# Kernel tuning notes

Hardware: AMD Instinct MI355X
Metric: run time of the kernel (lower is better)

## Reference

```python
import jax, jax.numpy as jnp
import numpy as np


def setup_inputs() -> dict:
    key = jax.random.key(0)
    k1, k2 = jax.random.split(key)
    querry_emb = jax.random.normal(k1, (4096, 1024), dtype=jnp.float32)
    traj_emb = jax.random.normal(k2, (8192, 1024), dtype=jnp.float32)
    return {"querry_emb": querry_emb, "traj_emb": traj_emb}


def reference(querry_emb, traj_emb):
    # Cosine-similarity score: (Q K^T) / (|q| outer |k|)  -> [Nq, Nk]
    q_norm = jnp.sqrt(jnp.sum(querry_emb * querry_emb, axis=1))  # [Nq]
    k_norm = jnp.sqrt(jnp.sum(traj_emb * traj_emb, axis=1))      # [Nk]
    score = jnp.einsum('qd,kd->qk', querry_emb, traj_emb) / (q_norm[:, None] * k_norm[None, :])
    # Softmax over key axis (torch dim=1 on [Nq, Nk])
    atten = jax.nn.softmax(score, axis=1)
    # Context: weighted sum of values (traj_emb)
    context = jnp.einsum('qk,kd->qd', atten, traj_emb)
    return context
```

## Files before the change

### kernel.cpp

```cpp
#include <hip/hip_runtime.h>

#define NQ 4096
#define NK 8192
#define DIM 1024

typedef __attribute__((ext_vector_type(8))) short short8;
typedef __attribute__((ext_vector_type(4))) float floatx4;
typedef unsigned int u32;
typedef __attribute__((address_space(3))) u32 lds_u32;
typedef __attribute__((address_space(1))) const u32 glb_u32;

__device__ __forceinline__ void gload_lds16(const void* g, void* l) {
    __builtin_amdgcn_global_load_lds((glb_u32*)g, (lds_u32*)l, 16, 0, 0);
}

__device__ __forceinline__ unsigned short f32_bf16(float f) {
    unsigned int u = __float_as_uint(f);
    u += 0x7fff + ((u >> 16) & 1);
    return (unsigned short)(u >> 16);
}

__device__ __forceinline__ void tile_body(const unsigned short* A0,
                                          const unsigned short* B0,
                                          int ar, int br,
                                          floatx4 (&acc)[8][4]) {
    short8 a[4], b[4];
#pragma unroll
    for (int nj = 0; nj < 4; ++nj)
        b[nj] = *(const short8*)&B0[br + nj * 512];
#pragma unroll
    for (int mi = 0; mi < 4; ++mi)
        a[mi] = *(const short8*)&A0[ar + mi * 512];
    __builtin_amdgcn_s_setprio(1);
#pragma unroll
    for (int mi = 0; mi < 4; ++mi)
#pragma unroll
        for (int nj = 0; nj < 4; ++nj)
            acc[mi][nj] = __builtin_amdgcn_mfma_f32_16x16x32_bf16(b[nj], a[mi], acc[mi][nj], 0, 0, 0);
    __builtin_amdgcn_s_setprio(0);
#pragma unroll
    for (int mi = 0; mi < 4; ++mi)
        a[mi] = *(const short8*)&A0[ar + 2048 + mi * 512];
    __builtin_amdgcn_s_setprio(1);
#pragma unroll
    for (int mi = 0; mi < 4; ++mi)
#pragma unroll
        for (int nj = 0; nj < 4; ++nj)
            acc[4 + mi][nj] = __builtin_amdgcn_mfma_f32_16x16x32_bf16(b[nj], a[mi], acc[4 + mi][nj], 0, 0, 0);
    __builtin_amdgcn_s_setprio(0);
}

__global__ void prep_q_zero(const float* __restrict__ Q,
                            unsigned short* __restrict__ Qb,
                            float* __restrict__ inv_qn,
                            float* __restrict__ lsum,
                            float* __restrict__ out_zero) {
    int wave = threadIdx.x >> 6;
    int lane = threadIdx.x & 63;
    int row  = blockIdx.x * 4 + wave;
    const float* r = Q + (size_t)row * DIM;
    float s = 0.f;
#pragma unroll
    for (int c = 0; c < 4; ++c) {
        float4 f = *(const float4*)(r + c * 256 + lane * 4);
        s += f.x * f.x + f.y * f.y + f.z * f.z + f.w * f.w;
        ushort4 b;
        b.x = f32_bf16(f.x); b.y = f32_bf16(f.y);
        b.z = f32_bf16(f.z); b.w = f32_bf16(f.w);
        *(ushort4*)(Qb + (size_t)row * DIM + c * 256 + lane * 4) = b;
    }
#pragma unroll
    for (int off = 32; off > 0; off >>= 1) s += __shfl_xor(s, off);
    if (lane == 0) inv_qn[row] = 1.0f / sqrtf(s);

    float4 z = make_float4(0.f, 0.f, 0.f, 0.f);
    if (out_zero) {
#pragma unroll
        for (int c = 0; c < 4; ++c)
            *(float4*)(out_zero + (size_t)blockIdx.x * 4096 + c * 1024 + threadIdx.x * 4) = z;
    }
    if (blockIdx.x < 4)
        *(float4*)(lsum + blockIdx.x * 1024 + threadIdx.x * 4) = z;
}

__global__ void prep_norm_cvt(const float* __restrict__ src,
                              unsigned short* __restrict__ dst,
                              float* __restrict__ inv_norm) {
    int wave = threadIdx.x >> 6;
    int lane = threadIdx.x & 63;
    int row  = blockIdx.x * 4 + wave;
    const float* r = src + (size_t)row * DIM;
    float s = 0.f;
#pragma unroll
    for (int c = 0; c < 4; ++c) {
        float4 f = *(const float4*)(r + c * 256 + lane * 4);
        s += f.x * f.x + f.y * f.y + f.z * f.z + f.w * f.w;
        ushort4 b;
        b.x = f32_bf16(f.x); b.y = f32_bf16(f.y);
        b.z = f32_bf16(f.z); b.w = f32_bf16(f.w);
        *(ushort4*)(dst + (size_t)row * DIM + c * 256 + lane * 4) = b;
    }
#pragma unroll
    for (int off = 32; off > 0; off >>= 1) s += __shfl_xor(s, off);
    if (lane == 0) inv_norm[row] = 1.0f / sqrtf(s);
}

__global__ void transpose_cvt(const float* __restrict__ K,
                              unsigned short* __restrict__ Kt) {
    __shared__ float t[64][65];
    int kn0 = blockIdx.x * 64, d0 = blockIdx.y * 64;
    int tid = threadIdx.x;
    int r  = tid >> 4;
    int c4 = (tid & 15) * 4;
#pragma unroll
    for (int s = 0; s < 4; ++s) {
        int kk = s * 16 + r;
        float4 f = *(const float4*)(K + (size_t)(kn0 + kk) * DIM + d0 + c4);
        t[kk][c4 + 0] = f.x; t[kk][c4 + 1] = f.y;
        t[kk][c4 + 2] = f.z; t[kk][c4 + 3] = f.w;
    }
    __syncthreads();
#pragma unroll
    for (int s = 0; s < 4; ++s) {
        int dd = s * 16 + r;
        ushort4 b;
        b.x = f32_bf16(t[c4 + 0][dd]);
        b.y = f32_bf16(t[c4 + 1][dd]);
        b.z = f32_bf16(t[c4 + 2][dd]);
        b.w = f32_bf16(t[c4 + 3][dd]);
        *(ushort4*)(Kt + (size_t)(d0 + dd) * NK + kn0 + c4) = b;
    }
}

__global__ __launch_bounds__(512, 2) void score_gemm(
        const unsigned short* __restrict__ Qb,
        const unsigned short* __restrict__ Kb,
        const float* __restrict__ inv_qn,
        const float* __restrict__ inv_kn,
        unsigned short* __restrict__ P,
        float* __restrict__ lsum) {
    __shared__ __align__(16) unsigned short A_lds[4][256 * 32];
    __shared__ __align__(16) unsigned short B_lds[4][256 * 32];

    int bid = blockIdx.x;
    int swz = (bid & 7) * 64 + (bid >> 3);
    int q0  = (swz & 15) * 256;
    int n0  = (swz >> 4) * 256;

    int tid  = threadIdx.x;
    int wave = tid >> 6, lane = tid & 63;
    int wm = wave >> 2, wn = wave & 3;
    int quad = lane >> 4, l16 = lane & 15;
    int rcol = (quad ^ ((l16 >> 1) & 3)) * 8;

    int schunk = ((tid & 3) ^ ((tid >> 3) & 3)) * 8;
    const unsigned short* gA = Qb + (size_t)(q0 + (tid >> 2)) * DIM + schunk;
    const unsigned short* gB = Kb + (size_t)(n0 + (tid >> 2)) * DIM + schunk;

#define STG(t1)                                                       \
    do {                                                              \
        const unsigned short* _ga = gA + (t1) * 32;                   \
        const unsigned short* _gb = gB + (t1) * 32;                   \
        unsigned short* _la = &A_lds[(t1) & 3][wave * 512];           \
        unsigned short* _lb = &B_lds[(t1) & 3][wave * 512];           \
        gload_lds16(_ga, _la);                                        \
        gload_lds16(_ga + (size_t)128 * DIM, _la + 4096);             \
        gload_lds16(_gb, _lb);                                        \
        gload_lds16(_gb + (size_t)128 * DIM, _lb + 4096);             \
    } while (0)

    floatx4 acc[8][4];
#pragma unroll
    for (int i = 0; i < 8; ++i)
#pragma unroll
        for (int j = 0; j < 4; ++j) acc[i][j] = (floatx4)(0.0f);

    const int ar = (wm * 128 + l16) * 32 + rcol;
    const int br = (wn * 64 + l16) * 32 + rcol;

    STG(0); STG(1); STG(2);

#pragma unroll 4
    for (int t = 0; t < 28; ++t) {
        asm volatile("s_waitcnt vmcnt(8)" ::: "memory");
        __builtin_amdgcn_s_barrier();
        STG(t + 3);
        tile_body(&A_lds[t & 3][0], &B_lds[t & 3][0], ar, br, acc);
    }
    asm volatile("s_waitcnt vmcnt(8)" ::: "memory");
    __builtin_amdgcn_s_barrier();
    STG(31);
    tile_body(&A_lds[0][0], &B_lds[0][0], ar, br, acc);
    asm volatile("s_waitcnt vmcnt(8)" ::: "memory");
    __builtin_amdgcn_s_barrier();
    tile_body(&A_lds[1][0], &B_lds[1][0], ar, br, acc);
    asm volatile("s_waitcnt vmcnt(4)" ::: "memory");
    __builtin_amdgcn_s_barrier();
    tile_body(&A_lds[2][0], &B_lds[2][0], ar, br, acc);
    asm volatile("s_waitcnt vmcnt(0)" ::: "memory");
    __builtin_amdgcn_s_barrier();
    tile_body(&A_lds[3][0], &B_lds[3][0], ar, br, acc);
#undef STG

#pragma unroll
    for (int i = 0; i < 8; ++i) {
        int qrow = q0 + wm * 128 + i * 16 + l16;
        float iqn = inv_qn[qrow];
        float rs = 0.f;
#pragma unroll
        for (int j = 0; j < 4; ++j) {
            int ncol = n0 + wn * 64 + j * 16 + quad * 4;
            float4 ik = *(const float4*)&inv_kn[ncol];
            float p0 = __expf(acc[i][j][0] * iqn * ik.x);
            float p1 = __expf(acc[i][j][1] * iqn * ik.y);
            float p2 = __expf(acc[i][j][2] * iqn * ik.z);
            float p3 = __expf(acc[i][j][3] * iqn * ik.w);
            ushort4 pb;
            pb.x = f32_bf16(p0); pb.y = f32_bf16(p1);
            pb.z = f32_bf16(p2); pb.w = f32_bf16(p3);
            *(ushort4*)&P[(size_t)qrow * NK + ncol] = pb;
            rs += p0 + p1 + p2 + p3;
        }
        rs += __shfl_xor(rs, 16);
        rs += __shfl_xor(rs, 32);
        if (quad == 0) atomicAdd(&lsum[qrow], rs);
    }
}

__global__ __launch_bounds__(512, 2) void ctx_gemm_st(
        const unsigned short* __restrict__ P,
        const unsigned short* __restrict__ Kt,
        float* __restrict__ part) {
    __shared__ __align__(16) unsigned short A_lds[4][256 * 32];
    __shared__ __align__(16) unsigned short B_lds[4][256 * 32];

    int bid = blockIdx.x;
    int swz = (bid & 7) * 32 + (bid >> 3);
    int z  = swz >> 6;
    int y  = (swz >> 2) & 15;
    int x  = swz & 3;
    int q0 = y * 256;
    int d0 = x * 256;
    int kbase = z * (NK / 4);

    int tid  = threadIdx.x;
    int wave = tid >> 6, lane = tid & 63;
    int wm = wave >> 2, wn = wave & 3;
    int quad = lane >> 4, l16 = lane & 15;
    int rcol = (quad ^ ((l16 >> 1) & 3)) * 8;

    int schunk = ((tid & 3) ^ ((tid >> 3) & 3)) * 8;
    const unsigned short* gA = P  + (size_t)(q0 + (tid >> 2)) * NK + kbase + schunk;
    const unsigned short* gB = Kt + (size_t)(d0 + (tid >> 2)) * NK + kbase + schunk;

#define STG(t1)                                                       \
    do {                                                              \
        const unsigned short* _ga = gA + (t1) * 32;                   \
        const unsigned short* _gb = gB + (t1) * 32;                   \
        unsigned short* _la = &A_lds[(t1) & 3][wave * 512];           \
        unsigned short* _lb = &B_lds[(t1) & 3][wave * 512];           \
        gload_lds16(_ga, _la);                                        \
        gload_lds16(_ga + (size_t)128 * NK, _la + 4096);              \
        gload_lds16(_gb, _lb);                                        \
        gload_lds16(_gb + (size_t)128 * NK, _lb + 4096);              \
    } while (0)

    floatx4 acc[8][4];
#pragma unroll
    for (int i = 0; i < 8; ++i)
#pragma unroll
        for (int j = 0; j < 4; ++j) acc[i][j] = (floatx4)(0.0f);

    const int ar = (wm * 128 + l16) * 32 + rcol;
    const int br = (wn * 64 + l16) * 32 + rcol;

    STG(0); STG(1); STG(2);

#pragma unroll 4
    for (int t = 0; t < 60; ++t) {
        asm volatile("s_waitcnt vmcnt(8)" ::: "memory");
        __builtin_amdgcn_s_barrier();
        STG(t + 3);
        tile_body(&A_lds[t & 3][0], &B_lds[t & 3][0], ar, br, acc);
    }
    asm volatile("s_waitcnt vmcnt(8)" ::: "memory");
    __builtin_amdgcn_s_barrier();
    STG(63);
    tile_body(&A_lds[0][0], &B_lds[0][0], ar, br, acc);
    asm volatile("s_waitcnt vmcnt(8)" ::: "memory");
    __builtin_amdgcn_s_barrier();
    tile_body(&A_lds[1][0], &B_lds[1][0], ar, br, acc);
    asm volatile("s_waitcnt vmcnt(4)" ::: "memory");
    __builtin_amdgcn_s_barrier();
    tile_body(&A_lds[2][0], &B_lds[2][0], ar, br, acc);
    asm volatile("s_waitcnt vmcnt(0)" ::: "memory");
    __builtin_amdgcn_s_barrier();
    tile_body(&A_lds[3][0], &B_lds[3][0], ar, br, acc);
#undef STG

    float* pslice = part + (size_t)z * NQ * DIM;
#pragma unroll
    for (int i = 0; i < 8; ++i) {
        int qrow = q0 + wm * 128 + i * 16 + l16;
#pragma unroll
        for (int j = 0; j < 4; ++j) {
            int dcol = d0 + wn * 64 + j * 16 + quad * 4;
            float4 v;
            v.x = acc[i][j][0]; v.y = acc[i][j][1];
            v.z = acc[i][j][2]; v.w = acc[i][j][3];
            *(float4*)&pslice[(size_t)qrow * DIM + dcol] = v;
        }
    }
}

__global__ void reduce_out(const float* __restrict__ part,
                           const float* __restrict__ lsum,
                           float* __restrict__ out) {
    size_t idx = ((size_t)blockIdx.x * 256 + threadIdx.x) * 4;
    int q = (int)(idx >> 10);
    float inv = 1.0f / lsum[q];
    const size_t S = (size_t)NQ * DIM;
    float4 s0 = *(const float4*)(part + idx);
    float4 s1 = *(const float4*)(part + S + idx);
    float4 s2 = *(const float4*)(part + 2 * S + idx);
    float4 s3 = *(const float4*)(part + 3 * S + idx);
    float4 o;
    o.x = (s0.x + s1.x + s2.x + s3.x) * inv;
    o.y = (s0.y + s1.y + s2.y + s3.y) * inv;
    o.z = (s0.z + s1.z + s2.z + s3.z) * inv;
    o.w = (s0.w + s1.w + s2.w + s3.w) * inv;
    *(float4*)(out + idx) = o;
}

__global__ void ctx_gemm(const unsigned short* __restrict__ P,
                         const unsigned short* __restrict__ Kt,
                         const float* __restrict__ lsum,
                         float* __restrict__ out) {
    __shared__ __align__(16) unsigned short As[128 * 32];
    __shared__ __align__(16) unsigned short Bs[128 * 32];
    int id = blockIdx.x;
    int r8 = id & 7;
    int t  = id >> 3;
    int x  = t & 7;
    int g  = ((t >> 3) << 3) | r8;
    int y  = g & 31;
    int z  = g >> 5;
    int q0 = y * 128;
    int d0 = x * 128;
    int kbase = z * (NK / 4);

    int tid = threadIdx.x;
    int wave = tid >> 6, lane = tid & 63;
    int wm = wave >> 1, wn = wave & 1;
    int quad = lane >> 4, l16 = lane & 15;

    int srow   = wave * 32 + (lane >> 2);
    int schunk = (((lane & 3) ^ ((lane >> 3) & 3))) * 8;
    const unsigned short* gA0 = P + (size_t)(q0 + srow) * NK + kbase + schunk;
    const unsigned short* gA1 = gA0 + (size_t)16 * NK;
    const unsigned short* gB0 = Kt + (size_t)(d0 + srow) * NK + kbase + schunk;
    const unsigned short* gB1 = gB0 + (size_t)16 * NK;
    unsigned short* lA0 = As + wave * 32 * 32;
    unsigned short* lA1 = lA0 + 16 * 32;
    unsigned short* lB0 = Bs + wave * 32 * 32;
    unsigned short* lB1 = lB0 + 16 * 32;

    int rcol = (quad ^ ((l16 >> 1) & 3)) * 8;

    floatx4 acc[4][4];
#pragma unroll
    for (int i = 0; i < 4; ++i)
#pragma unroll
        for (int j = 0; j < 4; ++j) acc[i][j] = (floatx4)(0.0f);

    for (int kb = 0; kb < (NK / 4) / 32; ++kb) {
        int k0 = kb * 32;
        __syncthreads();
        gload_lds16(gA0 + k0, lA0);
        gload_lds16(gA1 + k0, lA1);
        gload_lds16(gB0 + k0, lB0);
        gload_lds16(gB1 + k0, lB1);
        __syncthreads();
        short8 a[4], b[4];
#pragma unroll
        for (int i = 0; i < 4; ++i)
            a[i] = *(const short8*)&As[(wm * 64 + i * 16 + l16) * 32 + rcol];
#pragma unroll
        for (int j = 0; j < 4; ++j)
            b[j] = *(const short8*)&Bs[(wn * 64 + j * 16 + l16) * 32 + rcol];
#pragma unroll
        for (int i = 0; i < 4; ++i)
#pragma unroll
            for (int j = 0; j < 4; ++j)
                acc[i][j] = __builtin_amdgcn_mfma_f32_16x16x32_bf16(a[i], b[j], acc[i][j], 0, 0, 0);
    }

#pragma unroll
    for (int i = 0; i < 4; ++i) {
        float invl[4];
#pragma unroll
        for (int r = 0; r < 4; ++r)
            invl[r] = 1.0f / lsum[q0 + wm * 64 + i * 16 + quad * 4 + r];
#pragma unroll
        for (int j = 0; j < 4; ++j) {
#pragma unroll
            for (int r = 0; r < 4; ++r) {
                int qrow = q0 + wm * 64 + i * 16 + quad * 4 + r;
                int dcol = d0 + wn * 64 + j * 16 + l16;
                atomicAdd(&out[(size_t)qrow * DIM + dcol], acc[i][j][r] * invl[r]);
            }
        }
    }
}

__global__ void fused_fallback(const float* __restrict__ Q,
                               const float* __restrict__ K,
                               float* __restrict__ out) {
    int wave = threadIdx.x >> 6, lane = threadIdx.x & 63;
    int q0 = blockIdx.x * 16 + wave * 4;
    float qv[4][16], acc[4][16], iqn[4], ls[4];
#pragma unroll
    for (int r = 0; r < 4; ++r) {
        float s = 0.f;
#pragma unroll
        for (int c = 0; c < 4; ++c) {
            float4 f = *(const float4*)(Q + (size_t)(q0 + r) * DIM + c * 256 + lane * 4);
            qv[r][c * 4 + 0] = f.x; qv[r][c * 4 + 1] = f.y;
            qv[r][c * 4 + 2] = f.z; qv[r][c * 4 + 3] = f.w;
            s += f.x * f.x + f.y * f.y + f.z * f.z + f.w * f.w;
        }
#pragma unroll
        for (int off = 32; off > 0; off >>= 1) s += __shfl_xor(s, off);
        iqn[r] = 1.0f / sqrtf(s);
        ls[r] = 0.f;
#pragma unroll
        for (int t = 0; t < 16; ++t) acc[r][t] = 0.f;
    }
    for (int k = 0; k < NK; ++k) {
        const float* kr = K + (size_t)k * DIM;
        float kv[16], ss = 0.f;
#pragma unroll
        for (int c = 0; c < 4; ++c) {
            float4 f = *(const float4*)(kr + c * 256 + lane * 4);
            kv[c * 4 + 0] = f.x; kv[c * 4 + 1] = f.y;
            kv[c * 4 + 2] = f.z; kv[c * 4 + 3] = f.w;
            ss += f.x * f.x + f.y * f.y + f.z * f.z + f.w * f.w;
        }
        float d0 = 0.f, d1 = 0.f, d2 = 0.f, d3 = 0.f;
#pragma unroll
        for (int t = 0; t < 16; ++t) {
            d0 += qv[0][t] * kv[t]; d1 += qv[1][t] * kv[t];
            d2 += qv[2][t] * kv[t]; d3 += qv[3][t] * kv[t];
        }
#pragma unroll
        for (int off = 32; off > 0; off >>= 1) {
            ss += __shfl_xor(ss, off);
            d0 += __shfl_xor(d0, off); d1 += __shfl_xor(d1, off);
            d2 += __shfl_xor(d2, off); d3 += __shfl_xor(d3, off);
        }
        float ikn = 1.0f / sqrtf(ss);
        float p0 = __expf(d0 * iqn[0] * ikn), p1 = __expf(d1 * iqn[1] * ikn);
        float p2 = __expf(d2 * iqn[2] * ikn), p3 = __expf(d3 * iqn[3] * ikn);
        ls[0] += p0; ls[1] += p1; ls[2] += p2; ls[3] += p3;
#pragma unroll
        for (int t = 0; t < 16; ++t) {
            acc[0][t] += p0 * kv[t]; acc[1][t] += p1 * kv[t];
            acc[2][t] += p2 * kv[t]; acc[3][t] += p3 * kv[t];
        }
    }
#pragma unroll
    for (int r = 0; r < 4; ++r) {
        float inv = 1.0f / ls[r];
#pragma unroll
        for (int c = 0; c < 4; ++c) {
            float4 o;
            o.x = acc[r][c * 4 + 0] * inv; o.y = acc[r][c * 4 + 1] * inv;
            o.z = acc[r][c * 4 + 2] * inv; o.w = acc[r][c * 4 + 3] * inv;
            *(float4*)(out + (size_t)(q0 + r) * DIM + c * 256 + lane * 4) = o;
        }
    }
}

extern "C" void kernel_launch(void* const* d_in, const int* in_sizes, int n_in,
                              void* d_out, int out_size, void* d_ws, size_t ws_size,
                              hipStream_t stream) {
    const float* Q = (const float*)d_in[0];
    const float* K = (const float*)d_in[1];
    float* out = (float*)d_out;
    char* ws = (char*)d_ws;

    const size_t REQ_T1 = ((size_t)152u << 20) + 65536;
    const size_t REQ_T2 = ((size_t)88u << 20) + 65536;

    if (ws_size >= REQ_T1) {
        unsigned short* Kt = (unsigned short*)(ws);
        unsigned short* Qb = (unsigned short*)(ws);
        unsigned short* Kb = (unsigned short*)(ws + (size_t)(8u << 20));
        unsigned short* P  = (unsigned short*)(ws + (size_t)(24u << 20));
        float* part   = (float*)(ws + (size_t)(88u << 20));
        float* inv_qn = (float*)(ws + (size_t)(152u << 20));
        float* inv_kn = (float*)(ws + (size_t)(152u << 20) + 16384);
        float* lsum   = (float*)(ws + (size_t)(152u << 20) + 49152);

        prep_q_zero<<<NQ / 4, 256, 0, stream>>>(Q, Qb, inv_qn, lsum, nullptr);
        prep_norm_cvt<<<NK / 4, 256, 0, stream>>>(K, Kb, inv_kn);
        score_gemm<<<512, 512, 0, stream>>>(Qb, Kb, inv_qn, inv_kn, P, lsum);
        transpose_cvt<<<dim3(NK / 64, DIM / 64), 256, 0, stream>>>(K, Kt);
        ctx_gemm_st<<<256, 512, 0, stream>>>(P, Kt, part);
        reduce_out<<<NQ * DIM / 1024, 256, 0, stream>>>(part, lsum, out);
    } else if (ws_size >= REQ_T2) {
        unsigned short* Kt = (unsigned short*)(ws);
        unsigned short* Qb = (unsigned short*)(ws);
        unsigned short* Kb = (unsigned short*)(ws + (size_t)(8u << 20));
        unsigned short* P  = (unsigned short*)(ws + (size_t)(24u << 20));
        float* inv_qn = (float*)(ws + (size_t)(88u << 20));
        float* inv_kn = (float*)(ws + (size_t)(88u << 20) + 16384);
        float* lsum   = (float*)(ws + (size_t)(88u << 20) + 49152);

        prep_q_zero<<<NQ / 4, 256, 0, stream>>>(Q, Qb, inv_qn, lsum, out);
        prep_norm_cvt<<<NK / 4, 256, 0, stream>>>(K, Kb, inv_kn);
        score_gemm<<<512, 512, 0, stream>>>(Qb, Kb, inv_qn, inv_kn, P, lsum);
        transpose_cvt<<<dim3(NK / 64, DIM / 64), 256, 0, stream>>>(K, Kt);
        ctx_gemm<<<1024, 256, 0, stream>>>(P, Kt, lsum, out);
    } else {
        fused_fallback<<<NQ / 16, 256, 0, stream>>>(Q, K, out);
    }
}
```

Baseline: 263.7 us.

## Shrink GEMM block tiles to 128x256 with double buffering and more blocks

Score and context GEMMs move from 256x256 tiles with a 4-stage LDS pipeline to 128x256 tiles with a 2-stage pipeline. This halves accumulator registers and LDS per block, allowing launch bounds of 4 blocks per CU and doubling the grid sizes. The goal is more occupancy and better CU load balance. The trade-offs are lower data reuse per tile, more global traffic for B, and a full vmcnt(0) wait each iteration that shortens prefetch depth.

```diff
diff --git a/kernel.cpp b/kernel.cpp
--- a/kernel.cpp
+++ b/kernel.cpp
@@ -18,36 +18,6 @@
     unsigned int u = __float_as_uint(f);
     u += 0x7fff + ((u >> 16) & 1);
     return (unsigned short)(u >> 16);
-}
-
-__device__ __forceinline__ void tile_body(const unsigned short* A0,
-                                          const unsigned short* B0,
-                                          int ar, int br,
-                                          floatx4 (&acc)[8][4]) {
-    short8 a[4], b[4];
-#pragma unroll
-    for (int nj = 0; nj < 4; ++nj)
-        b[nj] = *(const short8*)&B0[br + nj * 512];
-#pragma unroll
-    for (int mi = 0; mi < 4; ++mi)
-        a[mi] = *(const short8*)&A0[ar + mi * 512];
-    __builtin_amdgcn_s_setprio(1);
-#pragma unroll
-    for (int mi = 0; mi < 4; ++mi)
-#pragma unroll
-        for (int nj = 0; nj < 4; ++nj)
-            acc[mi][nj] = __builtin_amdgcn_mfma_f32_16x16x32_bf16(b[nj], a[mi], acc[mi][nj], 0, 0, 0);
-    __builtin_amdgcn_s_setprio(0);
-#pragma unroll
-    for (int mi = 0; mi < 4; ++mi)
-        a[mi] = *(const short8*)&A0[ar + 2048 + mi * 512];
-    __builtin_amdgcn_s_setprio(1);
-#pragma unroll
-    for (int mi = 0; mi < 4; ++mi)
-#pragma unroll
-        for (int nj = 0; nj < 4; ++nj)
-            acc[4 + mi][nj] = __builtin_amdgcn_mfma_f32_16x16x32_bf16(b[nj], a[mi], acc[4 + mi][nj], 0, 0, 0);
-    __builtin_amdgcn_s_setprio(0);
 }
 
 __global__ void prep_q_zero(const float* __restrict__ Q,
@@ -132,20 +102,20 @@
     }
 }
 
-__global__ __launch_bounds__(512, 2) void score_gemm(
+__global__ __launch_bounds__(512, 4) void score_gemm(
         const unsigned short* __restrict__ Qb,
         const unsigned short* __restrict__ Kb,
         const float* __restrict__ inv_qn,
         const float* __restrict__ inv_kn,
         unsigned short* __restrict__ P,
         float* __restrict__ lsum) {
-    __shared__ __align__(16) unsigned short A_lds[4][256 * 32];
-    __shared__ __align__(16) unsigned short B_lds[4][256 * 32];
+    __shared__ __align__(16) unsigned short A_lds[2][128 * 32];
+    __shared__ __align__(16) unsigned short B_lds[2][256 * 32];
 
     int bid = blockIdx.x;
-    int swz = (bid & 7) * 64 + (bid >> 3);
-    int q0  = (swz & 15) * 256;
-    int n0  = (swz >> 4) * 256;
+    int swz = (bid & 7) * 128 + (bid >> 3);
+    int q0  = (swz & 31) * 128;
+    int n0  = (swz >> 5) * 256;
 
     int tid  = threadIdx.x;
     int wave = tid >> 6, lane = tid & 63;
@@ -159,52 +129,49 @@
 
 #define STG(t1)                                                       \
     do {                                                              \
-        const unsigned short* _ga = gA + (t1) * 32;                   \
-        const unsigned short* _gb = gB + (t1) * 32;                   \
-        unsigned short* _la = &A_lds[(t1) & 3][wave * 512];           \
-        unsigned short* _lb = &B_lds[(t1) & 3][wave * 512];           \
-        gload_lds16(_ga, _la);                                        \
-        gload_lds16(_ga + (size_t)128 * DIM, _la + 4096);             \
-        gload_lds16(_gb, _lb);                                        \
-        gload_lds16(_gb + (size_t)128 * DIM, _lb + 4096);             \
+        gload_lds16(gA + (t1) * 32, &A_lds[(t1) & 1][wave * 512]);    \
+        gload_lds16(gB + (t1) * 32, &B_lds[(t1) & 1][wave * 512]);    \
+        gload_lds16(gB + (size_t)128 * DIM + (t1) * 32,               \
+                    &B_lds[(t1) & 1][wave * 512 + 4096]);             \
     } while (0)
 
-    floatx4 acc[8][4];
-#pragma unroll
-    for (int i = 0; i < 8; ++i)
+    floatx4 acc[4][4];
+#pragma unroll
+    for (int i = 0; i < 4; ++i)
 #pragma unroll
         for (int j = 0; j < 4; ++j) acc[i][j] = (floatx4)(0.0f);
 
-    const int ar = (wm * 128 + l16) * 32 + rcol;
+    const int ar = (wm * 64 + l16) * 32 + rcol;
     const int br = (wn * 64 + l16) * 32 + rcol;
-
-    STG(0); STG(1); STG(2);
-
-#pragma unroll 4
-    for (int t = 0; t < 28; ++t) {
-        asm volatile("s_waitcnt vmcnt(8)" ::: "memory");
+    const int NT = DIM / 32;
+
+    STG(0);
+#pragma unroll 2
+    for (int t = 0; t < NT; ++t) {
+        asm volatile("s_waitcnt vmcnt(0)" ::: "memory");
         __builtin_amdgcn_s_barrier();
-        STG(t + 3);
-        tile_body(&A_lds[t & 3][0], &B_lds[t & 3][0], ar, br, acc);
-    }
-    asm volatile("s_waitcnt vmcnt(8)" ::: "memory");
-    __builtin_amdgcn_s_barrier();
-    STG(31);
-    tile_body(&A_lds[0][0], &B_lds[0][0], ar, br, acc);
-    asm volatile("s_waitcnt vmcnt(8)" ::: "memory");
-    __builtin_amdgcn_s_barrier();
-    tile_body(&A_lds[1][0], &B_lds[1][0], ar, br, acc);
-    asm volatile("s_waitcnt vmcnt(4)" ::: "memory");
-    __builtin_amdgcn_s_barrier();
-    tile_body(&A_lds[2][0], &B_lds[2][0], ar, br, acc);
-    asm volatile("s_waitcnt vmcnt(0)" ::: "memory");
-    __builtin_amdgcn_s_barrier();
-    tile_body(&A_lds[3][0], &B_lds[3][0], ar, br, acc);
+        if (t + 1 < NT) STG(t + 1);
+        const unsigned short* Ab = &A_lds[t & 1][0];
+        const unsigned short* Bb = &B_lds[t & 1][0];
+        short8 b[4];
+#pragma unroll
+        for (int nj = 0; nj < 4; ++nj)
+            b[nj] = *(const short8*)&Bb[br + nj * 512];
+        __builtin_amdgcn_s_setprio(1);
+#pragma unroll
+        for (int mi = 0; mi < 4; ++mi) {
+            short8 a = *(const short8*)&Ab[ar + mi * 512];
+#pragma unroll
+            for (int nj = 0; nj < 4; ++nj)
+                acc[mi][nj] = __builtin_amdgcn_mfma_f32_16x16x32_bf16(b[nj], a, acc[mi][nj], 0, 0, 0);
+        }
+        __builtin_amdgcn_s_setprio(0);
+    }
 #undef STG
 
 #pragma unroll
-    for (int i = 0; i < 8; ++i) {
-        int qrow = q0 + wm * 128 + i * 16 + l16;
+    for (int i = 0; i < 4; ++i) {
+        int qrow = q0 + wm * 64 + i * 16 + l16;
         float iqn = inv_qn[qrow];
         float rs = 0.f;
 #pragma unroll
@@ -227,19 +194,20 @@
     }
 }
 
-__global__ __launch_bounds__(512, 2) void ctx_gemm_st(
+__global__ __launch_bounds__(512, 4) void ctx_gemm_st(
         const unsigned short* __restrict__ P,
         const unsigned short* __restrict__ Kt,
         float* __restrict__ part) {
-    __shared__ __align__(16) unsigned short A_lds[4][256 * 32];
-    __shared__ __align__(16) unsigned short B_lds[4][256 * 32];
+    __shared__ __align__(16) unsigned short A_lds[2][128 * 32];
+    __shared__ __align__(16) unsigned short B_lds[2][256 * 32];
 
     int bid = blockIdx.x;
-    int swz = (bid & 7) * 32 + (bid >> 3);
-    int z  = swz >> 6;
-    int y  = (swz >> 2) & 15;
-    int x  = swz & 3;
-    int q0 = y * 256;
+    int swz = (bid & 7) * 64 + (bid >> 3);
+    int z  = swz >> 7;
+    int rem = swz & 127;
+    int y  = rem >> 2;
+    int x  = rem & 3;
+    int q0 = y * 128;
     int d0 = x * 256;
     int kbase = z * (NK / 4);
 
@@ -255,53 +223,50 @@
 
 #define STG(t1)                                                       \
     do {                                                              \
-        const unsigned short* _ga = gA + (t1) * 32;                   \
-        const unsigned short* _gb = gB + (t1) * 32;                   \
-        unsigned short* _la = &A_lds[(t1) & 3][wave * 512];           \
-        unsigned short* _lb = &B_lds[(t1) & 3][wave * 512];           \
-        gload_lds16(_ga, _la);                                        \
-        gload_lds16(_ga + (size_t)128 * NK, _la + 4096);              \
-        gload_lds16(_gb, _lb);                                        \
-        gload_lds16(_gb + (size_t)128 * NK, _lb + 4096);              \
+        gload_lds16(gA + (t1) * 32, &A_lds[(t1) & 1][wave * 512]);    \
+        gload_lds16(gB + (t1) * 32, &B_lds[(t1) & 1][wave * 512]);    \
+        gload_lds16(gB + (size_t)128 * NK + (t1) * 32,                \
+                    &B_lds[(t1) & 1][wave * 512 + 4096]);             \
     } while (0)
 
-    floatx4 acc[8][4];
-#pragma unroll
-    for (int i = 0; i < 8; ++i)
+    floatx4 acc[4][4];
+#pragma unroll
+    for (int i = 0; i < 4; ++i)
 #pragma unroll
         for (int j = 0; j < 4; ++j) acc[i][j] = (floatx4)(0.0f);
 
-    const int ar = (wm * 128 + l16) * 32 + rcol;
+    const int ar = (wm * 64 + l16) * 32 + rcol;
     const int br = (wn * 64 + l16) * 32 + rcol;
-
-    STG(0); STG(1); STG(2);
-
-#pragma unroll 4
-    for (int t = 0; t < 60; ++t) {
-        asm volatile("s_waitcnt vmcnt(8)" ::: "memory");
+    const int NT = (NK / 4) / 32;
+
+    STG(0);
+#pragma unroll 2
+    for (int t = 0; t < NT; ++t) {
+        asm volatile("s_waitcnt vmcnt(0)" ::: "memory");
         __builtin_amdgcn_s_barrier();
-        STG(t + 3);
-        tile_body(&A_lds[t & 3][0], &B_lds[t & 3][0], ar, br, acc);
-    }
-    asm volatile("s_waitcnt vmcnt(8)" ::: "memory");
-    __builtin_amdgcn_s_barrier();
-    STG(63);
-    tile_body(&A_lds[0][0], &B_lds[0][0], ar, br, acc);
-    asm volatile("s_waitcnt vmcnt(8)" ::: "memory");
-    __builtin_amdgcn_s_barrier();
-    tile_body(&A_lds[1][0], &B_lds[1][0], ar, br, acc);
-    asm volatile("s_waitcnt vmcnt(4)" ::: "memory");
-    __builtin_amdgcn_s_barrier();
-    tile_body(&A_lds[2][0], &B_lds[2][0], ar, br, acc);
-    asm volatile("s_waitcnt vmcnt(0)" ::: "memory");
-    __builtin_amdgcn_s_barrier();
-    tile_body(&A_lds[3][0], &B_lds[3][0], ar, br, acc);
+        if (t + 1 < NT) STG(t + 1);
+        const unsigned short* Ab = &A_lds[t & 1][0];
+        const unsigned short* Bb = &B_lds[t & 1][0];
+        short8 b[4];
+#pragma unroll
+        for (int nj = 0; nj < 4; ++nj)
+            b[nj] = *(const short8*)&Bb[br + nj * 512];
+        __builtin_amdgcn_s_setprio(1);
+#pragma unroll
+        for (int mi = 0; mi < 4; ++mi) {
+            short8 a = *(const short8*)&Ab[ar + mi * 512];
+#pragma unroll
+            for (int nj = 0; nj < 4; ++nj)
+                acc[mi][nj] = __builtin_amdgcn_mfma_f32_16x16x32_bf16(b[nj], a, acc[mi][nj], 0, 0, 0);
+        }
+        __builtin_amdgcn_s_setprio(0);
+    }
 #undef STG
 
     float* pslice = part + (size_t)z * NQ * DIM;
 #pragma unroll
-    for (int i = 0; i < 8; ++i) {
-        int qrow = q0 + wm * 128 + i * 16 + l16;
+    for (int i = 0; i < 4; ++i) {
+        int qrow = q0 + wm * 64 + i * 16 + l16;
 #pragma unroll
         for (int j = 0; j < 4; ++j) {
             int dcol = d0 + wn * 64 + j * 16 + quad * 4;
@@ -504,9 +469,9 @@
 
         prep_q_zero<<<NQ / 4, 256, 0, stream>>>(Q, Qb, inv_qn, lsum, nullptr);
         prep_norm_cvt<<<NK / 4, 256, 0, stream>>>(K, Kb, inv_kn);
-        score_gemm<<<512, 512, 0, stream>>>(Qb, Kb, inv_qn, inv_kn, P, lsum);
+        score_gemm<<<1024, 512, 0, stream>>>(Qb, Kb, inv_qn, inv_kn, P, lsum);
         transpose_cvt<<<dim3(NK / 64, DIM / 64), 256, 0, stream>>>(K, Kt);
-        ctx_gemm_st<<<256, 512, 0, stream>>>(P, Kt, part);
+        ctx_gemm_st<<<512, 512, 0, stream>>>(P, Kt, part);
         reduce_out<<<NQ * DIM / 1024, 256, 0, stream>>>(part, lsum, out);
     } else if (ws_size >= REQ_T2) {
         unsigned short* Kt = (unsigned short*)(ws);
@@ -519,7 +484,7 @@
 
         prep_q_zero<<<NQ / 4, 256, 0, stream>>>(Q, Qb, inv_qn, lsum, out);
         prep_norm_cvt<<<NK / 4, 256, 0, stream>>>(K, Kb, inv_kn);
-        score_gemm<<<512, 512, 0, stream>>>(Qb, Kb, inv_qn, inv_kn, P, lsum);
+        score_gemm<<<1024, 512, 0, stream>>>(Qb, Kb, inv_qn, inv_kn, P, lsum);
         transpose_cvt<<<dim3(NK / 64, DIM / 64), 256, 0, stream>>>(K, Kt);
         ctx_gemm<<<1024, 256, 0, stream>>>(P, Kt, lsum, out);
     } else {
```

Result: no change. 263.3 us (-0.2%).
